# Optimization experiments

Measured on AMD Instinct MI355X. Metric: run time of the kernel, lower is better.

## Reference

```python
import jax, jax.numpy as jnp
import numpy as np


def setup_inputs() -> dict:
    key = jax.random.key(0)
    ks = jax.random.split(key, 7)
    B, T, C, H = 8, 2048, 2048, 128
    x = jax.random.normal(ks[0], (B, T, C), dtype=jnp.float32)
    Wq = jax.random.normal(ks[1], (C, H), dtype=jnp.float32) * (C ** -0.5)
    bq = jax.random.normal(ks[2], (H,), dtype=jnp.float32) * 0.02
    Wk = jax.random.normal(ks[3], (C, H), dtype=jnp.float32) * (C ** -0.5)
    bk = jax.random.normal(ks[4], (H,), dtype=jnp.float32) * 0.02
    Wv = jax.random.normal(ks[5], (C, H), dtype=jnp.float32) * (C ** -0.5)
    bv = jax.random.normal(ks[6], (H,), dtype=jnp.float32) * 0.02
    return {"x": x, "Wq": Wq, "bq": bq, "Wk": Wk, "bk": bk, "Wv": Wv, "bv": bv}


def reference(x, Wq, bq, Wk, bk, Wv, bv):
    # Single-head causal self-attention (dropout in eval mode = identity).
    B, T, C = x.shape
    H = Wq.shape[1]
    Q = jnp.einsum("btc,ch->bth", x, Wq) + bq  # [B,T,H]
    K = jnp.einsum("btc,ch->bth", x, Wk) + bk
    V = jnp.einsum("btc,ch->bth", x, Wv) + bv
    scale = H ** -0.5
    wei = jnp.einsum("bth,bsh->bts", Q, K) * scale  # [B,T,T]
    causal = jnp.tril(jnp.ones((T, T), dtype=bool))
    wei = jnp.where(causal, wei, -jnp.inf)
    wei = jax.nn.softmax(wei, axis=-1)
    out = jnp.einsum("bts,bsh->bth", wei, V)  # [B,T,H]
    return out
```

## Files before the change

kernel.cpp:

```cpp
#include <hip/hip_runtime.h>

typedef float f32x4 __attribute__((ext_vector_type(4)));
typedef short short8 __attribute__((ext_vector_type(8)));
typedef unsigned short ushort8 __attribute__((ext_vector_type(8)));

#define AS1 __attribute__((address_space(1)))
#define AS3 __attribute__((address_space(3)))

#define WS_Q  786432
#define WS_K  2883584
#define WS_VT 4980736

__device__ __forceinline__ unsigned short f2bf(float x) {
    unsigned u = __float_as_uint(x);
    u += 0x7FFFu + ((u >> 16) & 1u);
    return (unsigned short)(u >> 16);
}

__device__ __forceinline__ short8 cvt8(float4 lo, float4 hi) {
    union { unsigned u[4]; short8 s; } r;
    asm("v_cvt_pk_bf16_f32 %0, %1, %2" : "=v"(r.u[0]) : "v"(lo.x), "v"(lo.y));
    asm("v_cvt_pk_bf16_f32 %0, %1, %2" : "=v"(r.u[1]) : "v"(lo.z), "v"(lo.w));
    asm("v_cvt_pk_bf16_f32 %0, %1, %2" : "=v"(r.u[2]) : "v"(hi.x), "v"(hi.y));
    asm("v_cvt_pk_bf16_f32 %0, %1, %2" : "=v"(r.u[3]) : "v"(hi.z), "v"(hi.w));
    return r.s;
}

__device__ __forceinline__ int swz128(int row, int cbyte) {
    return row * 128 + (cbyte ^ ((row & 7) << 4));
}

__global__ __launch_bounds__(256) void wt_kernel(const float* __restrict__ Wq,
        const float* __restrict__ Wk, const float* __restrict__ Wv,
        unsigned short* __restrict__ ws) {
    __shared__ __align__(16) unsigned short tile[64][136];
    int mat = blockIdx.x >> 5, ct = blockIdx.x & 31;
    const float* W = (mat == 0) ? Wq : ((mat == 1) ? Wk : Wv);
    int cbase = ct * 64;
    int tid = threadIdx.x;
#pragma unroll
    for (int p = 0; p < 8; p++) {
        int fidx = p * 256 + tid;
        int row = fidx >> 5;
        int c4 = (fidx & 31) << 2;
        float4 v = *(const float4*)&W[(size_t)(cbase + row) * 128 + c4];
        tile[row][c4 + 0] = f2bf(v.x);
        tile[row][c4 + 1] = f2bf(v.y);
        tile[row][c4 + 2] = f2bf(v.z);
        tile[row][c4 + 3] = f2bf(v.w);
    }
    __syncthreads();
    int h = tid >> 1, seg = tid & 1;
    int ks = ct * 2 + seg;
    unsigned short* base = ws + mat * 262144 + ks * 4096 + h * 32;
    int hx = (h >> 1) & 3;
#pragma unroll
    for (int u = 0; u < 4; u++) {
        ushort8 pk;
#pragma unroll
        for (int e = 0; e < 8; e++) pk[e] = tile[seg * 32 + u * 8 + e][h];
        *(ushort8*)(base + ((u ^ hx) << 3)) = pk;
    }
}

__global__ __launch_bounds__(256, 3) void qkv_kernel(const float* __restrict__ x,
        const float* __restrict__ bq, const float* __restrict__ bk,
        const float* __restrict__ bv, unsigned short* __restrict__ ws) {
    __shared__ __align__(16) char lds[3][16384];
    int bid = blockIdx.x;
    int g = bid / 24, j = bid - g * 24;
    int matrix = j >> 3;
    int mt = g * 8 + (j & 7);
    const unsigned short* WTt = ws + matrix * 262144;
    const float* x0 = x + (size_t)mt * 64 * 2048;
    int tid = threadIdx.x, lane = tid & 63, wid = tid >> 6;
    int lr = lane & 15, lg = lane >> 4;
    int m0 = (wid >> 1) * 32, n0 = (wid & 1) * 64;

    int rA = tid >> 3;
    int pA = tid & 7;
    int cA = pA ^ (rA & 7);
    const float* aSrc0 = x0 + (size_t)rA * 2048 + cA * 4;
    const float* aSrc1 = aSrc0 + (size_t)32 * 2048;
    int aDst0 = tid * 16, aDst1 = tid * 16 + 4096;

    int bDst0 = 8192 + tid * 16, bDst1 = 8192 + 4096 + tid * 16;

    int aOff00, aOff01, aOff10, aOff11, bOff0, bOff1, bOff2, bOff3;
    {
        int r0 = m0 + lr, r1 = m0 + 16 + lr;
        aOff00 = r0 * 128 + (((lg * 2 + 0) ^ (r0 & 7)) << 4);
        aOff01 = r0 * 128 + (((lg * 2 + 1) ^ (r0 & 7)) << 4);
        aOff10 = r1 * 128 + (((lg * 2 + 0) ^ (r1 & 7)) << 4);
        aOff11 = r1 * 128 + (((lg * 2 + 1) ^ (r1 & 7)) << 4);
        int h0 = n0 + lr, h1 = n0 + 16 + lr, h2 = n0 + 32 + lr, h3 = n0 + 48 + lr;
        bOff0 = 8192 + h0 * 64 + ((lg ^ ((h0 >> 1) & 3)) << 4);
        bOff1 = 8192 + h1 * 64 + ((lg ^ ((h1 >> 1) & 3)) << 4);
        bOff2 = 8192 + h2 * 64 + ((lg ^ ((h2 >> 1) & 3)) << 4);
        bOff3 = 8192 + h3 * 64 + ((lg ^ ((h3 >> 1) & 3)) << 4);
    }

    f32x4 acc[2][4];
#pragma unroll
    for (int i = 0; i < 2; i++)
#pragma unroll
        for (int j3 = 0; j3 < 4; j3++) acc[i][j3] = (f32x4){0.f, 0.f, 0.f, 0.f};

#define ISSUE(BUF, T) do { \
        char* Lb_ = &lds[BUF][0]; \
        const float* a0_ = aSrc0 + (size_t)(T) * 32; \
        const float* a1_ = aSrc1 + (size_t)(T) * 32; \
        __builtin_amdgcn_global_load_lds((const AS1 unsigned*)a0_, \
            (AS3 unsigned*)(Lb_ + aDst0), 16, 0, 0); \
        __builtin_amdgcn_global_load_lds((const AS1 unsigned*)a1_, \
            (AS3 unsigned*)(Lb_ + aDst1), 16, 0, 0); \
        const unsigned short* bs_ = WTt + (size_t)(T) * 4096 + tid * 8; \
        __builtin_amdgcn_global_load_lds((const AS1 unsigned*)bs_, \
            (AS3 unsigned*)(Lb_ + bDst0), 16, 0, 0); \
        __builtin_amdgcn_global_load_lds((const AS1 unsigned*)(bs_ + 2048), \
            (AS3 unsigned*)(Lb_ + bDst1), 16, 0, 0); \
    } while (0)

#define BODY(U, T, STAGE, WAITN, BAR) do { \
        if (STAGE) ISSUE(((U) + 2) % 3, (T) + 2); \
        const char* Lb_ = &lds[U][0]; \
        float4 alo0 = *(const float4*)(Lb_ + aOff00); \
        float4 ahi0 = *(const float4*)(Lb_ + aOff01); \
        float4 alo1 = *(const float4*)(Lb_ + aOff10); \
        float4 ahi1 = *(const float4*)(Lb_ + aOff11); \
        short8 b0 = *(const short8*)(Lb_ + bOff0); \
        short8 b1 = *(const short8*)(Lb_ + bOff1); \
        short8 b2 = *(const short8*)(Lb_ + bOff2); \
        short8 b3 = *(const short8*)(Lb_ + bOff3); \
        short8 a0 = cvt8(alo0, ahi0); \
        short8 a1 = cvt8(alo1, ahi1); \
        __builtin_amdgcn_s_setprio(1); \
        acc[0][0] = __builtin_amdgcn_mfma_f32_16x16x32_bf16(a0, b0, acc[0][0], 0, 0, 0); \
        acc[0][1] = __builtin_amdgcn_mfma_f32_16x16x32_bf16(a0, b1, acc[0][1], 0, 0, 0); \
        acc[0][2] = __builtin_amdgcn_mfma_f32_16x16x32_bf16(a0, b2, acc[0][2], 0, 0, 0); \
        acc[0][3] = __builtin_amdgcn_mfma_f32_16x16x32_bf16(a0, b3, acc[0][3], 0, 0, 0); \
        acc[1][0] = __builtin_amdgcn_mfma_f32_16x16x32_bf16(a1, b0, acc[1][0], 0, 0, 0); \
        acc[1][1] = __builtin_amdgcn_mfma_f32_16x16x32_bf16(a1, b1, acc[1][1], 0, 0, 0); \
        acc[1][2] = __builtin_amdgcn_mfma_f32_16x16x32_bf16(a1, b2, acc[1][2], 0, 0, 0); \
        acc[1][3] = __builtin_amdgcn_mfma_f32_16x16x32_bf16(a1, b3, acc[1][3], 0, 0, 0); \
        __builtin_amdgcn_s_setprio(0); \
        if ((WAITN) == 4)      { asm volatile("s_waitcnt vmcnt(4)" ::: "memory"); } \
        else if ((WAITN) == 0) { asm volatile("s_waitcnt vmcnt(0)" ::: "memory"); } \
        if (BAR) { \
            __builtin_amdgcn_s_barrier(); \
            asm volatile("" ::: "memory");    \
        } \
    } while (0)

    ISSUE(0, 0);
    ISSUE(1, 1);
    asm volatile("s_waitcnt vmcnt(4)" ::: "memory");
    __builtin_amdgcn_s_barrier();
    asm volatile("" ::: "memory");

    for (int t3 = 0; t3 < 20; t3++) {
        int T0 = t3 * 3;
        BODY(0, T0 + 0, true, 4, true);
        BODY(1, T0 + 1, true, 4, true);
        BODY(2, T0 + 2, true, 4, true);
    }
    BODY(0, 60, true,  4,  true);
    BODY(1, 61, true,  4,  true);
    BODY(2, 62, false, 0,  true);
    BODY(0, 63, false, -1, false);
#undef BODY
#undef ISSUE

    const float* bias = (matrix == 0) ? bq : ((matrix == 1) ? bk : bv);
    float bb[4];
#pragma unroll
    for (int j3 = 0; j3 < 4; j3++) bb[j3] = bias[n0 + j3 * 16 + lr];
    if (matrix < 2) {
        unsigned short* outp = ws + ((matrix == 0) ? WS_Q : WS_K);
        float sc = (matrix == 0) ? 0.08838834764831845f : 1.0f;
#pragma unroll
        for (int i = 0; i < 2; i++)
#pragma unroll
            for (int j3 = 0; j3 < 4; j3++) {
                int h = n0 + j3 * 16 + lr;
#pragma unroll
                for (int r = 0; r < 4; r++) {
                    size_t t = (size_t)mt * 64 + m0 + i * 16 + (lg << 2) + r;
                    outp[t * 128 + h] = f2bf((acc[i][j3][r] + bb[j3]) * sc);
                }
            }
    } else {
        __syncthreads();
        unsigned short* sm = (unsigned short*)&lds[0][0];
#pragma unroll
        for (int i = 0; i < 2; i++)
#pragma unroll
            for (int j3 = 0; j3 < 4; j3++) {
                int h = n0 + j3 * 16 + lr;
#pragma unroll
                for (int r = 0; r < 4; r++) {
                    int tl = m0 + i * 16 + (lg << 2) + r;
                    sm[tl * 136 + h] = f2bf(acc[i][j3][r] + bb[j3]);
                }
            }
        __syncthreads();
        int h = tid & 127, seg = tid >> 7;
        int b2 = mt >> 5;
        int tin = (mt & 31) * 64 + seg * 32;
        unsigned short* vt = ws + WS_VT + ((size_t)b2 * 128 + h) * 2048 + tin;
#pragma unroll
        for (int q4 = 0; q4 < 4; q4++) {
            ushort8 pk;
#pragma unroll
            for (int e = 0; e < 8; e++) pk[e] = sm[(seg * 32 + q4 * 8 + e) * 136 + h];
            *(ushort8*)(vt + q4 * 8) = pk;
        }
    }
}

__global__ __launch_bounds__(256, 2) void attn_kernel(const unsigned short* __restrict__ ws,
        float* __restrict__ out) {
    __shared__ __align__(16) float o_lds[4][32][128];
    __shared__ float ml[4][2][32];
    int b = blockIdx.x;
    int qi = 63 - (int)blockIdx.y;
    int qbase = qi * 32;
    int tid = threadIdx.x, lane = tid & 63, w = tid >> 6;
    int lr = lane & 15, lg = lane >> 4;
    const unsigned short* Qb = ws + WS_Q + (size_t)b * 2048 * 128;
    const unsigned short* Kb = ws + WS_K + (size_t)b * 2048 * 128;
    const unsigned short* Vt = ws + WS_VT + (size_t)b * 128 * 2048;
    char* p_lds = (char*)&o_lds[w][0][0];

    short8 qf[2][4];
#pragma unroll
    for (int i = 0; i < 2; i++)
#pragma unroll
        for (int kf = 0; kf < 4; kf++)
            qf[i][kf] = *(const short8*)&Qb[(size_t)(qbase + i * 16 + lr) * 128 + kf * 32 + lg * 8];

    f32x4 o[2][8];
#pragma unroll
    for (int i = 0; i < 2; i++)
#pragma unroll
        for (int jn = 0; jn < 8; jn++) o[i][jn] = (f32x4){0.f, 0.f, 0.f, 0.f};
    float mrow[2][4], lrow[2][4];
#pragma unroll
    for (int i = 0; i < 2; i++)
#pragma unroll
        for (int r = 0; r < 4; r++) { mrow[i][r] = -__builtin_inff(); lrow[i][r] = 0.f; }

    int ntiles = qi / 2 + 1;
    for (int ti = w; ti < ntiles; ti += 4) {
        int sb = ti * 64;
        f32x4 s[2][4];
#pragma unroll
        for (int i = 0; i < 2; i++)
#pragma unroll
            for (int nf = 0; nf < 4; nf++) s[i][nf] = (f32x4){0.f, 0.f, 0.f, 0.f};
        {
            short8 kb[4][4];
#pragma unroll
            for (int nf = 0; nf < 4; nf++)
#pragma unroll
                for (int kf = 0; kf < 4; kf++)
                    kb[nf][kf] = *(const short8*)&Kb[(size_t)(sb + nf * 16 + lr) * 128 + kf * 32 + lg * 8];
#pragma unroll
            for (int kf = 0; kf < 4; kf++)
#pragma unroll
                for (int i = 0; i < 2; i++)
#pragma unroll
                    for (int nf = 0; nf < 4; nf++)
                        s[i][nf] = __builtin_amdgcn_mfma_f32_16x16x32_bf16(qf[i][kf], kb[nf][kf], s[i][nf], 0, 0, 0);
        }
        if (sb + 63 > qbase) {
#pragma unroll
            for (int i = 0; i < 2; i++)
#pragma unroll
                for (int nf = 0; nf < 4; nf++)
#pragma unroll
                    for (int r = 0; r < 4; r++) {
                        int sg = sb + nf * 16 + lr;
                        int qg = qbase + i * 16 + (lg << 2) + r;
                        if (sg > qg) s[i][nf][r] = -__builtin_inff();
                    }
        }
        float alpha[2][4];
#pragma unroll
        for (int i = 0; i < 2; i++)
#pragma unroll
            for (int r = 0; r < 4; r++) {
                float pm = fmaxf(fmaxf(s[i][0][r], s[i][1][r]), fmaxf(s[i][2][r], s[i][3][r]));
                pm = fmaxf(pm, __shfl_xor(pm, 1));
                pm = fmaxf(pm, __shfl_xor(pm, 2));
                pm = fmaxf(pm, __shfl_xor(pm, 4));
                pm = fmaxf(pm, __shfl_xor(pm, 8));
                float mn = fmaxf(mrow[i][r], pm);
                alpha[i][r] = __expf(mrow[i][r] - mn);
                mrow[i][r] = mn;
            }
#pragma unroll
        for (int i = 0; i < 2; i++)
#pragma unroll
            for (int r = 0; r < 4; r++) {
                float rs = 0.f;
#pragma unroll
                for (int nf = 0; nf < 4; nf++) {
                    float p = __expf(s[i][nf][r] - mrow[i][r]);
                    s[i][nf][r] = p;
                    rs += p;
                }
                rs += __shfl_xor(rs, 1);
                rs += __shfl_xor(rs, 2);
                rs += __shfl_xor(rs, 4);
                rs += __shfl_xor(rs, 8);
                lrow[i][r] = lrow[i][r] * alpha[i][r] + rs;
            }
#pragma unroll
        for (int i = 0; i < 2; i++)
#pragma unroll
            for (int jn = 0; jn < 8; jn++)
#pragma unroll
                for (int r = 0; r < 4; r++) o[i][jn][r] *= alpha[i][r];
#pragma unroll
        for (int i = 0; i < 2; i++)
#pragma unroll
            for (int nf = 0; nf < 4; nf++)
#pragma unroll
                for (int r = 0; r < 4; r++) {
                    int row = i * 16 + (lg << 2) + r;
                    int cb2 = (nf * 16 + lr) * 2;
                    *(unsigned short*)(p_lds + swz128(row, cb2)) = f2bf(s[i][nf][r]);
                }
        asm volatile("s_waitcnt lgkmcnt(0)" ::: "memory");
        short8 pa[2][2];
#pragma unroll
        for (int i = 0; i < 2; i++)
#pragma unroll
            for (int kf = 0; kf < 2; kf++)
                pa[i][kf] = *(const short8*)(p_lds + swz128(i * 16 + lr, kf * 64 + lg * 16));
        short8 vb[8][2];
#pragma unroll
        for (int nf = 0; nf < 8; nf++)
#pragma unroll
            for (int kf = 0; kf < 2; kf++)
                vb[nf][kf] = *(const short8*)&Vt[(size_t)(nf * 16 + lr) * 2048 + sb + kf * 32 + lg * 8];
#pragma unroll
        for (int i = 0; i < 2; i++)
#pragma unroll
            for (int nf = 0; nf < 8; nf++)
#pragma unroll
                for (int kf = 0; kf < 2; kf++)
                    o[i][nf] = __builtin_amdgcn_mfma_f32_16x16x32_bf16(pa[i][kf], vb[nf][kf], o[i][nf], 0, 0, 0);
    }
#pragma unroll
    for (int i = 0; i < 2; i++)
#pragma unroll
        for (int r = 0; r < 4; r++) {
            int q = i * 16 + (lg << 2) + r;
            ml[w][0][q] = mrow[i][r];
            ml[w][1][q] = lrow[i][r];
        }
    asm volatile("s_waitcnt lgkmcnt(0)" ::: "memory");
#pragma unroll
    for (int i = 0; i < 2; i++)
#pragma unroll
        for (int jn = 0; jn < 8; jn++)
#pragma unroll
            for (int r = 0; r < 4; r++)
                o_lds[w][i * 16 + (lg << 2) + r][jn * 16 + lr] = o[i][jn][r];
    __syncthreads();
    int q = tid >> 3, h0 = (tid & 7) << 4;
    float mg = fmaxf(fmaxf(ml[0][0][q], ml[1][0][q]), fmaxf(ml[2][0][q], ml[3][0][q]));
    float scw[4], den = 0.f;
#pragma unroll
    for (int w4 = 0; w4 < 4; w4++) {
        scw[w4] = __expf(ml[w4][0][q] - mg);
        den += scw[w4] * ml[w4][1][q];
    }
    float inv = 1.0f / den;
    float* op = out + ((size_t)b * 2048 + qbase + q) * 128 + h0;
#pragma unroll
    for (int jj = 0; jj < 4; jj++) {
        f32x4 a4 = (f32x4){0.f, 0.f, 0.f, 0.f};
#pragma unroll
        for (int w4 = 0; w4 < 4; w4++) {
            f32x4 v = *(const f32x4*)&o_lds[w4][q][h0 + jj * 4];
            a4 += scw[w4] * v;
        }
        a4 *= inv;
        *(f32x4*)(op + jj * 4) = a4;
    }
}

extern "C" void kernel_launch(void* const* d_in, const int* in_sizes, int n_in,
                              void* d_out, int out_size, void* d_ws, size_t ws_size,
                              hipStream_t stream) {
    (void)in_sizes; (void)n_in; (void)out_size; (void)ws_size;
    const float* x  = (const float*)d_in[0];
    const float* Wq = (const float*)d_in[1];
    const float* bq = (const float*)d_in[2];
    const float* Wk = (const float*)d_in[3];
    const float* bk = (const float*)d_in[4];
    const float* Wv = (const float*)d_in[5];
    const float* bv = (const float*)d_in[6];
    unsigned short* ws = (unsigned short*)d_ws;
    float* out = (float*)d_out;

    wt_kernel<<<96, 256, 0, stream>>>(Wq, Wk, Wv, ws);
    qkv_kernel<<<768, 256, 0, stream>>>(x, bq, bk, bv, ws);
    attn_kernel<<<dim3(8, 64), 256, 0, stream>>>(ws, out);
}
```

Measured before the change: 110.8 us.

## Fuse Q/K/V projections into one block per 64-row strip

```diff
diff --git a/kernel.cpp b/kernel.cpp
--- a/kernel.cpp
+++ b/kernel.cpp
@@ -52,7 +52,7 @@
     __syncthreads();
     int h = tid >> 1, seg = tid & 1;
     int ks = ct * 2 + seg;
-    unsigned short* base = ws + mat * 262144 + ks * 4096 + h * 32;
+    unsigned short* base = ws + ks * 12288 + mat * 4096 + h * 32;
     int hx = (h >> 1) & 3;
 #pragma unroll
     for (int u = 0; u < 4; u++) {
@@ -63,92 +63,98 @@
     }
 }
 
-__global__ __launch_bounds__(256, 3) void qkv_kernel(const float* __restrict__ x,
+__global__ __launch_bounds__(512) void qkv_kernel(const float* __restrict__ x,
         const float* __restrict__ bq, const float* __restrict__ bk,
         const float* __restrict__ bv, unsigned short* __restrict__ ws) {
-    __shared__ __align__(16) char lds[3][16384];
-    int bid = blockIdx.x;
-    int g = bid / 24, j = bid - g * 24;
-    int matrix = j >> 3;
-    int mt = g * 8 + (j & 7);
-    const unsigned short* WTt = ws + matrix * 262144;
-    const float* x0 = x + (size_t)mt * 64 * 2048;
-    int tid = threadIdx.x, lane = tid & 63, wid = tid >> 6;
+    __shared__ __align__(16) char lds[98304];
+    int strip = blockIdx.x;
+    const float* x0 = x + (size_t)strip * 64 * 2048;
+    int tid = threadIdx.x, lane = tid & 63, w = tid >> 6;
     int lr = lane & 15, lg = lane >> 4;
-    int m0 = (wid >> 1) * 32, n0 = (wid & 1) * 64;
-
-    int rA = tid >> 3;
-    int pA = tid & 7;
+    int h = w * 16 + lr;
+
+    float bb0 = bq[h], bb1 = bk[h], bb2 = bv[h];
+    asm volatile("" : "+v"(bb0), "+v"(bb1), "+v"(bb2));
+    asm volatile("s_waitcnt vmcnt(0)" ::: "memory");
+
+    int rA = tid >> 3, pA = tid & 7;
     int cA = pA ^ (rA & 7);
-    const float* aSrc0 = x0 + (size_t)rA * 2048 + cA * 4;
-    const float* aSrc1 = aSrc0 + (size_t)32 * 2048;
-    int aDst0 = tid * 16, aDst1 = tid * 16 + 4096;
-
-    int bDst0 = 8192 + tid * 16, bDst1 = 8192 + 4096 + tid * 16;
-
-    int aOff00, aOff01, aOff10, aOff11, bOff0, bOff1, bOff2, bOff3;
-    {
-        int r0 = m0 + lr, r1 = m0 + 16 + lr;
-        aOff00 = r0 * 128 + (((lg * 2 + 0) ^ (r0 & 7)) << 4);
-        aOff01 = r0 * 128 + (((lg * 2 + 1) ^ (r0 & 7)) << 4);
-        aOff10 = r1 * 128 + (((lg * 2 + 0) ^ (r1 & 7)) << 4);
-        aOff11 = r1 * 128 + (((lg * 2 + 1) ^ (r1 & 7)) << 4);
-        int h0 = n0 + lr, h1 = n0 + 16 + lr, h2 = n0 + 32 + lr, h3 = n0 + 48 + lr;
-        bOff0 = 8192 + h0 * 64 + ((lg ^ ((h0 >> 1) & 3)) << 4);
-        bOff1 = 8192 + h1 * 64 + ((lg ^ ((h1 >> 1) & 3)) << 4);
-        bOff2 = 8192 + h2 * 64 + ((lg ^ ((h2 >> 1) & 3)) << 4);
-        bOff3 = 8192 + h3 * 64 + ((lg ^ ((h3 >> 1) & 3)) << 4);
-    }
-
-    f32x4 acc[2][4];
-#pragma unroll
-    for (int i = 0; i < 2; i++)
-#pragma unroll
-        for (int j3 = 0; j3 < 4; j3++) acc[i][j3] = (f32x4){0.f, 0.f, 0.f, 0.f};
+    const float* aSrc = x0 + (size_t)rA * 2048 + cA * 4;
+    int aDst = tid * 16;
+    const unsigned short* Bsrc = ws + tid * 8;
+
+    int aOff[4][2], bOff[3];
+#pragma unroll
+    for (int i = 0; i < 4; i++) {
+        int r = i * 16 + lr;
+#pragma unroll
+        for (int e = 0; e < 2; e++)
+            aOff[i][e] = r * 128 + (((2 * lg + e) ^ (r & 7)) << 4);
+    }
+#pragma unroll
+    for (int j = 0; j < 3; j++) {
+        int R = j * 128 + h;
+        bOff[j] = R * 64 + ((lg ^ ((R >> 1) & 3)) << 4);
+    }
+
+    f32x4 acc[4][3];
+#pragma unroll
+    for (int i = 0; i < 4; i++)
+#pragma unroll
+        for (int j = 0; j < 3; j++) acc[i][j] = (f32x4){0.f, 0.f, 0.f, 0.f};
 
 #define ISSUE(BUF, T) do { \
-        char* Lb_ = &lds[BUF][0]; \
-        const float* a0_ = aSrc0 + (size_t)(T) * 32; \
-        const float* a1_ = aSrc1 + (size_t)(T) * 32; \
-        __builtin_amdgcn_global_load_lds((const AS1 unsigned*)a0_, \
-            (AS3 unsigned*)(Lb_ + aDst0), 16, 0, 0); \
-        __builtin_amdgcn_global_load_lds((const AS1 unsigned*)a1_, \
-            (AS3 unsigned*)(Lb_ + aDst1), 16, 0, 0); \
-        const unsigned short* bs_ = WTt + (size_t)(T) * 4096 + tid * 8; \
+        char* Ab_ = lds + (BUF) * 8192; \
+        __builtin_amdgcn_global_load_lds((const AS1 unsigned*)(aSrc + (size_t)(T) * 32), \
+            (AS3 unsigned*)(Ab_ + aDst), 16, 0, 0); \
+        char* Bb_ = lds + 24576 + (BUF) * 24576 + tid * 16; \
+        const unsigned short* bs_ = Bsrc + (size_t)(T) * 12288; \
         __builtin_amdgcn_global_load_lds((const AS1 unsigned*)bs_, \
-            (AS3 unsigned*)(Lb_ + bDst0), 16, 0, 0); \
-        __builtin_amdgcn_global_load_lds((const AS1 unsigned*)(bs_ + 2048), \
-            (AS3 unsigned*)(Lb_ + bDst1), 16, 0, 0); \
+            (AS3 unsigned*)Bb_, 16, 0, 0); \
+        __builtin_amdgcn_global_load_lds((const AS1 unsigned*)(bs_ + 4096), \
+            (AS3 unsigned*)(Bb_ + 8192), 16, 0, 0); \
+        __builtin_amdgcn_global_load_lds((const AS1 unsigned*)(bs_ + 8192), \
+            (AS3 unsigned*)(Bb_ + 16384), 16, 0, 0); \
     } while (0)
 
 #define BODY(U, T, STAGE, WAITN, BAR) do { \
         if (STAGE) ISSUE(((U) + 2) % 3, (T) + 2); \
-        const char* Lb_ = &lds[U][0]; \
-        float4 alo0 = *(const float4*)(Lb_ + aOff00); \
-        float4 ahi0 = *(const float4*)(Lb_ + aOff01); \
-        float4 alo1 = *(const float4*)(Lb_ + aOff10); \
-        float4 ahi1 = *(const float4*)(Lb_ + aOff11); \
-        short8 b0 = *(const short8*)(Lb_ + bOff0); \
-        short8 b1 = *(const short8*)(Lb_ + bOff1); \
-        short8 b2 = *(const short8*)(Lb_ + bOff2); \
-        short8 b3 = *(const short8*)(Lb_ + bOff3); \
-        short8 a0 = cvt8(alo0, ahi0); \
-        short8 a1 = cvt8(alo1, ahi1); \
+        const char* Ab_ = lds + (U) * 8192; \
+        const char* Bb_ = lds + 24576 + (U) * 24576; \
+        float4 al0 = *(const float4*)(Ab_ + aOff[0][0]); \
+        float4 ah0 = *(const float4*)(Ab_ + aOff[0][1]); \
+        float4 al1 = *(const float4*)(Ab_ + aOff[1][0]); \
+        float4 ah1 = *(const float4*)(Ab_ + aOff[1][1]); \
+        float4 al2 = *(const float4*)(Ab_ + aOff[2][0]); \
+        float4 ah2 = *(const float4*)(Ab_ + aOff[2][1]); \
+        float4 al3 = *(const float4*)(Ab_ + aOff[3][0]); \
+        float4 ah3 = *(const float4*)(Ab_ + aOff[3][1]); \
+        short8 b0 = *(const short8*)(Bb_ + bOff[0]); \
+        short8 b1 = *(const short8*)(Bb_ + bOff[1]); \
+        short8 b2 = *(const short8*)(Bb_ + bOff[2]); \
+        short8 a0 = cvt8(al0, ah0); \
+        short8 a1 = cvt8(al1, ah1); \
+        short8 a2 = cvt8(al2, ah2); \
+        short8 a3 = cvt8(al3, ah3); \
         __builtin_amdgcn_s_setprio(1); \
         acc[0][0] = __builtin_amdgcn_mfma_f32_16x16x32_bf16(a0, b0, acc[0][0], 0, 0, 0); \
+        acc[1][0] = __builtin_amdgcn_mfma_f32_16x16x32_bf16(a1, b0, acc[1][0], 0, 0, 0); \
+        acc[2][0] = __builtin_amdgcn_mfma_f32_16x16x32_bf16(a2, b0, acc[2][0], 0, 0, 0); \
+        acc[3][0] = __builtin_amdgcn_mfma_f32_16x16x32_bf16(a3, b0, acc[3][0], 0, 0, 0); \
         acc[0][1] = __builtin_amdgcn_mfma_f32_16x16x32_bf16(a0, b1, acc[0][1], 0, 0, 0); \
+        acc[1][1] = __builtin_amdgcn_mfma_f32_16x16x32_bf16(a1, b1, acc[1][1], 0, 0, 0); \
+        acc[2][1] = __builtin_amdgcn_mfma_f32_16x16x32_bf16(a2, b1, acc[2][1], 0, 0, 0); \
+        acc[3][1] = __builtin_amdgcn_mfma_f32_16x16x32_bf16(a3, b1, acc[3][1], 0, 0, 0); \
         acc[0][2] = __builtin_amdgcn_mfma_f32_16x16x32_bf16(a0, b2, acc[0][2], 0, 0, 0); \
-        acc[0][3] = __builtin_amdgcn_mfma_f32_16x16x32_bf16(a0, b3, acc[0][3], 0, 0, 0); \
-        acc[1][0] = __builtin_amdgcn_mfma_f32_16x16x32_bf16(a1, b0, acc[1][0], 0, 0, 0); \
-        acc[1][1] = __builtin_amdgcn_mfma_f32_16x16x32_bf16(a1, b1, acc[1][1], 0, 0, 0); \
         acc[1][2] = __builtin_amdgcn_mfma_f32_16x16x32_bf16(a1, b2, acc[1][2], 0, 0, 0); \
-        acc[1][3] = __builtin_amdgcn_mfma_f32_16x16x32_bf16(a1, b3, acc[1][3], 0, 0, 0); \
+        acc[2][2] = __builtin_amdgcn_mfma_f32_16x16x32_bf16(a2, b2, acc[2][2], 0, 0, 0); \
+        acc[3][2] = __builtin_amdgcn_mfma_f32_16x16x32_bf16(a3, b2, acc[3][2], 0, 0, 0); \
         __builtin_amdgcn_s_setprio(0); \
         if ((WAITN) == 4)      { asm volatile("s_waitcnt vmcnt(4)" ::: "memory"); } \
         else if ((WAITN) == 0) { asm volatile("s_waitcnt vmcnt(0)" ::: "memory"); } \
         if (BAR) { \
             __builtin_amdgcn_s_barrier(); \
-            asm volatile("" ::: "memory");    \
+            asm volatile("" ::: "memory"); \
         } \
     } while (0)
 
@@ -171,51 +177,40 @@
 #undef BODY
 #undef ISSUE
 
-    const float* bias = (matrix == 0) ? bq : ((matrix == 1) ? bk : bv);
-    float bb[4];
-#pragma unroll
-    for (int j3 = 0; j3 < 4; j3++) bb[j3] = bias[n0 + j3 * 16 + lr];
-    if (matrix < 2) {
-        unsigned short* outp = ws + ((matrix == 0) ? WS_Q : WS_K);
-        float sc = (matrix == 0) ? 0.08838834764831845f : 1.0f;
-#pragma unroll
-        for (int i = 0; i < 2; i++)
-#pragma unroll
-            for (int j3 = 0; j3 < 4; j3++) {
-                int h = n0 + j3 * 16 + lr;
-#pragma unroll
-                for (int r = 0; r < 4; r++) {
-                    size_t t = (size_t)mt * 64 + m0 + i * 16 + (lg << 2) + r;
-                    outp[t * 128 + h] = f2bf((acc[i][j3][r] + bb[j3]) * sc);
-                }
-            }
-    } else {
-        __syncthreads();
-        unsigned short* sm = (unsigned short*)&lds[0][0];
-#pragma unroll
-        for (int i = 0; i < 2; i++)
-#pragma unroll
-            for (int j3 = 0; j3 < 4; j3++) {
-                int h = n0 + j3 * 16 + lr;
-#pragma unroll
-                for (int r = 0; r < 4; r++) {
-                    int tl = m0 + i * 16 + (lg << 2) + r;
-                    sm[tl * 136 + h] = f2bf(acc[i][j3][r] + bb[j3]);
-                }
-            }
-        __syncthreads();
-        int h = tid & 127, seg = tid >> 7;
-        int b2 = mt >> 5;
-        int tin = (mt & 31) * 64 + seg * 32;
-        unsigned short* vt = ws + WS_VT + ((size_t)b2 * 128 + h) * 2048 + tin;
-#pragma unroll
-        for (int q4 = 0; q4 < 4; q4++) {
-            ushort8 pk;
-#pragma unroll
-            for (int e = 0; e < 8; e++) pk[e] = sm[(seg * 32 + q4 * 8 + e) * 136 + h];
-            *(ushort8*)(vt + q4 * 8) = pk;
-        }
-    }
+    unsigned short* qout = ws + WS_Q;
+    unsigned short* kout = ws + WS_K;
+    const float sc = 0.08838834764831845f;
+#pragma unroll
+    for (int i = 0; i < 4; i++)
+#pragma unroll
+        for (int r = 0; r < 4; r++) {
+            int row = i * 16 + (lg << 2) + r;
+            size_t t = (size_t)strip * 64 + row;
+            qout[t * 128 + h] = f2bf((acc[i][0][r] + bb0) * sc);
+            kout[t * 128 + h] = f2bf(acc[i][1][r] + bb1);
+        }
+    __syncthreads();
+    unsigned short* sm = (unsigned short*)lds;
+#pragma unroll
+    for (int i = 0; i < 4; i++)
+#pragma unroll
+        for (int r = 0; r < 4; r++) {
+            int row = i * 16 + (lg << 2) + r;
+            sm[row * 136 + h] = f2bf(acc[i][2][r] + bb2);
+        }
+    __syncthreads();
+    int h2 = tid >> 2, part = tid & 3;
+    int batch = strip >> 5;
+    int tin = (strip & 31) * 64 + part * 16;
+    unsigned short* vt = ws + WS_VT + ((size_t)batch * 128 + h2) * 2048 + tin;
+    ushort8 pk0, pk1;
+#pragma unroll
+    for (int e = 0; e < 8; e++) {
+        pk0[e] = sm[(part * 16 + e) * 136 + h2];
+        pk1[e] = sm[(part * 16 + 8 + e) * 136 + h2];
+    }
+    *(ushort8*)vt = pk0;
+    *(ushort8*)(vt + 8) = pk1;
 }
 
 __global__ __launch_bounds__(256, 2) void attn_kernel(const unsigned short* __restrict__ ws,
@@ -408,6 +403,6 @@
     float* out = (float*)d_out;
 
     wt_kernel<<<96, 256, 0, stream>>>(Wq, Wk, Wv, ws);
-    qkv_kernel<<<768, 256, 0, stream>>>(x, bq, bk, bv, ws);
+    qkv_kernel<<<256, 512, 0, stream>>>(x, bq, bk, bv, ws);
     attn_kernel<<<dim3(8, 64), 256, 0, stream>>>(ws, out);
 }
```

After: 128.1 us. 1.16x slower.
